# Kernel optimization log

Measured on AMD Instinct MI355X. Metric: run time of the kernel, lower is better.

The kernel has to match this reference:

```python
import jax, jax.numpy as jnp
import numpy as np

K, N, NE, NI, MA, IN, B = 8, 512, 256, 256, 3, 128, 1024
H, UNFOLDS = 0.04, 6
DT = H / UNFOLDS
STATE = NE * MA + NI * MA + NE + NI + N  # 2560


def inv_softplus(x):
    return float(np.log(np.expm1(x)))


def piecewise_sigmoid(x, S_a=0.9, S_c=0.0):
    a = S_a / 2.0
    c = S_c
    k = 0.5 / (1.0 - 2.0 * a)  # = 5.0 for S_a=0.9
    x1, x2, x3, x4 = c + a - 1.0, c - a, c + a, c + 1.0 - a
    quad_rise = k * (x - x1) * (x - x1)
    linear = x - c + 0.5
    quad_cap = 1.0 - k * (x - x4) * (x - x4)
    out = jnp.where(x < x1, 0.0, quad_rise)
    out = jnp.where(x >= x2, linear, out)
    out = jnp.where(x > x3, quad_cap, out)
    out = jnp.where(x > x4, 1.0, out)
    return out


def setup_inputs():
    key = jax.random.key(0)
    ks = jax.random.split(key, 6)
    m = (jax.random.uniform(ks[0], (K, N, N)) > 0.5).astype(jnp.float32)  # sparsity masks
    W_raw = jax.random.normal(ks[1], (K, N, N)) * np.float32(np.sqrt(2.0 / N)) * m
    W_in = jax.random.normal(ks[2], (K, N, IN)) * 0.1
    lo, hi = inv_softplus(0.25), inv_softplus(10.0)
    taus = jnp.asarray([lo + (hi - lo) * ai / (MA - 1) for ai in range(MA)], dtype=jnp.float32)
    log_tau_a = jnp.tile(taus[None, None, :], (K, NE, 1))
    return {
        "inputs": jax.random.normal(ks[3], (B, IN), dtype=jnp.float32),
        "state": jax.random.uniform(ks[4], (K, B, STATE), dtype=jnp.float32),
        "W_raw": W_raw,
        "sparsity_masks": m,
        "W_in": W_in,
        "a_0": jnp.full((K, N), 0.35, jnp.float32),
        "log_tau_d": jnp.full((K, N), inv_softplus(0.1), jnp.float32),
        "log_tau_a_E": log_tau_a,
        "log_c_E": jnp.full((K, NE, MA), -3.0, jnp.float32),
        "c_0_E": jnp.zeros((K, NE, MA), jnp.float32),
        "log_tau_a_I": log_tau_a,
        "log_c_I": jnp.full((K, NI, MA), -3.0, jnp.float32),
        "c_0_I": jnp.zeros((K, NI, MA), jnp.float32),
        "log_tau_b_rec_E": jnp.full((K, NE), inv_softplus(1.0), jnp.float32),
        "log_tau_b_rel_E": jnp.full((K, NE), inv_softplus(0.25), jnp.float32),
        "log_tau_b_rec_I": jnp.full((K, NI), inv_softplus(1.0), jnp.float32),
        "log_tau_b_rel_I": jnp.full((K, NI), inv_softplus(0.25), jnp.float32),
        "readout_ids": jnp.zeros((K,), dtype=jnp.int32),  # 0=synaptic,1=rate,2=dendritic
    }


def _forward(inputs, state, W_raw, sparsity_masks, W_in, a_0, log_tau_d,
             log_tau_a_E, log_c_E, c_0_E, log_tau_a_I, log_c_I, c_0_I,
             log_tau_b_rec_E, log_tau_b_rel_E, log_tau_b_rec_I, log_tau_b_rel_I,
             readout_ids):
    sp = jax.nn.softplus
    # unpack flat state (K,B,STATE)
    i0 = NE * MA; i1 = i0 + NI * MA; i2 = i1 + NE; i3 = i2 + NI
    aE = state[:, :, :i0].reshape(K, B, NE, MA)
    aI = state[:, :, i0:i1].reshape(K, B, NI, MA)
    bE = state[:, :, i1:i2]          # (K,B,NE)
    bI = state[:, :, i2:i3]          # (K,B,NI)
    x = state[:, :, i3:]             # (K,B,N)
    # Dale-constrained effective recurrent weights
    W_pos = sp(W_raw)
    W_eff = jnp.concatenate([W_pos[:, :, :NE], -W_pos[:, :, NE:]], axis=2) * sparsity_masks
    # time-constant gains
    gx = DT / sp(log_tau_d)[:, None]                    # (K,1,N)
    gaE = DT / sp(log_tau_a_E)[:, None]                 # (K,1,NE,MA)
    gaI = DT / sp(log_tau_a_I)[:, None]
    cE = sp(log_c_E)[:, None]                           # (K,1,NE,MA)
    cI = sp(log_c_I)[:, None]
    grecE = (DT / sp(log_tau_b_rec_E))[:, None]         # (K,1,NE)
    grelE = (DT / sp(log_tau_b_rel_E))[:, None]
    grecI = (DT / sp(log_tau_b_rec_I))[:, None]
    grelI = (DT / sp(log_tau_b_rel_I))[:, None]
    in_cur = jnp.einsum('kni,bi->kbn', W_in, inputs)    # constant across unfolds

    def rate_syn(aE, aI, bE, bI, x):
        thr = a_0[:, None] + jnp.concatenate(
            [jnp.sum(aE + c_0_E[:, None], axis=-1),
             jnp.sum(aI + c_0_I[:, None], axis=-1)], axis=-1)
        r = piecewise_sigmoid(x - thr)                  # (K,B,N)
        s = r * jnp.concatenate([bE, bI], axis=-1)      # depression-scaled output
        return r, s

    def step(carry, _):
        aE, aI, bE, bI, x = carry
        r, s = rate_syn(aE, aI, bE, bI, x)
        rE, rI = r[..., :NE], r[..., NE:]
        syn = jnp.einsum('knm,kbm->kbn', W_eff, s) + in_cur
        x = (x + gx * syn) / (1.0 + gx)                 # semi-implicit Euler
        aE = (aE + gaE * cE * rE[..., None]) / (1.0 + gaE)
        aI = (aI + gaI * cI * rI[..., None]) / (1.0 + gaI)
        bE = (bE + grecE) / (1.0 + grecE + grelE * rE)
        bI = (bI + grecI) / (1.0 + grecI + grelI * rI)
        return (aE, aI, bE, bI, x), None

    (aE, aI, bE, bI, x), _ = jax.lax.scan(step, (aE, aI, bE, bI, x), None, length=UNFOLDS)
    r, s = rate_syn(aE, aI, bE, bI, x)
    rid = readout_ids[:, None, None]
    out = jnp.where(rid == 0, s, jnp.where(rid == 1, r, x))
    new_state = jnp.concatenate(
        [aE.reshape(K, B, -1), aI.reshape(K, B, -1), bE, bI, x], axis=-1)
    return out, new_state


def reference(inputs, state, W_raw, sparsity_masks, W_in, a_0, log_tau_d,
              log_tau_a_E, log_c_E, c_0_E, log_tau_a_I, log_c_I, c_0_I,
              log_tau_b_rec_E, log_tau_b_rel_E, log_tau_b_rec_I, log_tau_b_rel_I,
              readout_ids):
    return _forward(inputs, state, W_raw, sparsity_masks, W_in, a_0, log_tau_d,
                    log_tau_a_E, log_c_E, c_0_E, log_tau_a_I, log_c_I, c_0_I,
                    log_tau_b_rec_E, log_tau_b_rel_E, log_tau_b_rec_I, log_tau_b_rel_I,
                    readout_ids)
```

## Files before the change

kernel.cpp:

```cpp
#include <hip/hip_runtime.h>
#include <stdint.h>

#define K_ 8
#define N_ 512
#define NE_ 256
#define MA_ 3
#define IN_ 128
#define B_ 1024
#define STATE_ 2560
#define UNFOLDS_ 6
#define DT_ (0.04f / 6.0f)

typedef __attribute__((ext_vector_type(8))) short short8;
typedef __attribute__((ext_vector_type(4))) float floatx4;

__device__ __forceinline__ float b2f(uint16_t u) {
    union { uint32_t i; float f; } v; v.i = ((uint32_t)u) << 16; return v.f;
}
__device__ __forceinline__ uint16_t f2b(float f) {
    union { float f; uint32_t i; } v; v.f = f;
    uint32_t i = v.i;
    uint32_t r = i + 0x7FFFu + ((i >> 16) & 1u);
    return (uint16_t)(r >> 16);
}
__device__ __forceinline__ uint32_t pack2(uint16_t lo, uint16_t hi) {
    return (uint32_t)lo | ((uint32_t)hi << 16);
}
__device__ __forceinline__ float loadf(const void* p, size_t i, int f32) {
    return f32 ? ((const float*)p)[i] : b2f(((const uint16_t*)p)[i]);
}
__device__ __forceinline__ float ntloadf(const void* p, size_t i, int f32) {
    return f32 ? __builtin_nontemporal_load((const float*)p + i)
               : b2f(__builtin_nontemporal_load((const uint16_t*)p + i));
}
__device__ __forceinline__ float spf(float x) {
    return (x > 20.f) ? x : log1pf(expf(x));
}
__device__ __forceinline__ float psig(float x) {
    float t1 = x + 0.55f;
    float q1 = 5.f * t1 * t1;
    float t2 = x - 0.55f;
    float q2 = 1.f - 5.f * t2 * t2;
    float out = (x < -0.55f) ? 0.f : q1;
    out = (x >= -0.45f) ? (x + 0.5f) : out;
    out = (x > 0.45f) ? q2 : out;
    out = (x > 0.55f) ? 1.f : out;
    return out;
}

__global__ void srnn_detect_kernel(const uint16_t* canary, int* flag) {
    __shared__ int cnt;
    if (threadIdx.x == 0) cnt = 0;
    __syncthreads();
    int bad = 0;
    for (int i = threadIdx.x; i < 4096; i += 256) {
        uint16_t u = canary[i];
        int e = (u >> 7) & 0xFF;
        if (e >= 0xC0) bad++;
    }
    atomicAdd(&cnt, bad);
    __syncthreads();
    if (threadIdx.x == 0) flag[0] = (cnt >= 16) ? 1 : 0;
}

__global__ void srnn_params_kernel(
    const void* a0, const void* ltd,
    const void* ltaE, const void* lcE, const void* c0E,
    const void* ltaI, const void* lcI, const void* c0I,
    const void* lbrecE, const void* lbrelE,
    const void* lbrecI, const void* lbrelI,
    const int* flag, float* P)
{
    const int f = flag[0];
    int idx = blockIdx.x * 256 + threadIdx.x;
    if (idx >= K_ * N_) return;
    int n = idx & (N_ - 1);
    int k = idx >> 9;
    float gx = DT_ / spf(loadf(ltd, idx, f));
    float thr0 = loadf(a0, idx, f);

    const void *lta, *lc, *c0, *lbrec, *lbrel;
    int nn;
    if (n < NE_) { nn = n;        lta = ltaE; lc = lcE; c0 = c0E; lbrec = lbrecE; lbrel = lbrelE; }
    else         { nn = n - NE_;  lta = ltaI; lc = lcI; c0 = c0I; lbrec = lbrecI; lbrel = lbrelI; }
    int base3 = (k * NE_ + nn) * MA_;
    int base1 = k * NE_ + nn;

    float amul[3], ainv[3];
    #pragma unroll
    for (int j = 0; j < 3; ++j) {
        float ga = DT_ / spf(loadf(lta, base3 + j, f));
        float c  = spf(loadf(lc, base3 + j, f));
        amul[j] = ga * c;
        ainv[j] = 1.f / (1.f + ga);
        thr0 += loadf(c0, base3 + j, f);
    }
    float grec = DT_ / spf(loadf(lbrec, base1, f));
    float grel = DT_ / spf(loadf(lbrel, base1, f));

    const int KN = K_ * N_;
    P[0*KN + idx] = gx;
    P[1*KN + idx] = 1.f / (1.f + gx);
    P[2*KN + idx] = thr0;
    P[3*KN + idx] = grec;
    P[4*KN + idx] = grel;
    P[5*KN + idx] = amul[0]; P[6*KN + idx] = amul[1]; P[7*KN + idx] = amul[2];
    P[8*KN + idx] = ainv[0]; P[9*KN + idx] = ainv[1]; P[10*KN + idx] = ainv[2];
    P[11*KN + idx] = 1.f + grec;
}

__global__ __launch_bounds__(256) void srnn_wsw_kernel(
    const void* __restrict__ Wraw, const void* __restrict__ mask,
    const int* __restrict__ flag, uint16_t* __restrict__ Wsw)
{
    __shared__ float tile[16 * 516];
    const int f = flag[0];
    const int nt = blockIdx.x, k = blockIdx.y, t = threadIdx.x;
    const size_t base = (size_t)k * N_ * N_ + (size_t)nt * 16 * N_;
    #pragma unroll
    for (int i = 0; i < 32; ++i) {
        int idx = i * 256 + t;
        int row = idx >> 9, m = idx & 511;
        size_t gi = base + (size_t)row * N_ + m;
        float w = spf(ntloadf(Wraw, gi, f)) * ntloadf(mask, gi, f);
        if (m >= NE_) w = -w;
        tile[row * 516 + m] = w;
    }
    __syncthreads();
    uint16_t* outb = Wsw + ((size_t)k * 32 + nt) * (16 * 64 * 8);
    #pragma unroll
    for (int i = 0; i < 4; ++i) {
        int id = i * 256 + t;
        int ks = id >> 6, L = id & 63;
        int row = L & 15, quad = L >> 4;
        const float* src = &tile[row * 516 + ks * 32 + quad * 8];
        uint4 v;
        v.x = pack2(f2b(src[0]), f2b(src[1]));
        v.y = pack2(f2b(src[2]), f2b(src[3]));
        v.z = pack2(f2b(src[4]), f2b(src[5]));
        v.w = pack2(f2b(src[6]), f2b(src[7]));
        *(uint4*)(outb + (size_t)id * 8) = v;
    }
}

__global__ __launch_bounds__(256) void srnn_winsw_kernel(
    const void* __restrict__ Win, const int* __restrict__ flag,
    uint16_t* __restrict__ Winsw)
{
    __shared__ float tile[16 * 132];
    const int f = flag[0];
    const int nt = blockIdx.x, k = blockIdx.y, t = threadIdx.x;
    const size_t base = (size_t)k * N_ * IN_ + (size_t)nt * 16 * IN_;
    #pragma unroll
    for (int i = 0; i < 8; ++i) {
        int idx = i * 256 + t;
        int row = idx >> 7, c = idx & 127;
        tile[row * 132 + c] = ntloadf(Win, base + (size_t)row * IN_ + c, f);
    }
    __syncthreads();
    uint16_t* outb = Winsw + ((size_t)k * 32 + nt) * (4 * 64 * 8);
    {
        int id = t;
        int ks = id >> 6, L = id & 63;
        int row = L & 15, quad = L >> 4;
        const float* src = &tile[row * 132 + ks * 32 + quad * 8];
        uint4 v;
        v.x = pack2(f2b(src[0]), f2b(src[1]));
        v.y = pack2(f2b(src[2]), f2b(src[3]));
        v.z = pack2(f2b(src[4]), f2b(src[5]));
        v.w = pack2(f2b(src[6]), f2b(src[7]));
        *(uint4*)(outb + (size_t)id * 8) = v;
    }
}

__global__ __launch_bounds__(1024, 4)
void srnn_main_kernel(const void* __restrict__ state,
                      const void* __restrict__ inputs,
                      const uint16_t* __restrict__ Wsw,
                      const uint16_t* __restrict__ Winsw,
                      const float* __restrict__ P,
                      const int* __restrict__ readout,
                      const int* __restrict__ flag,
                      void* __restrict__ out)
{
    __shared__ __align__(16) uint16_t sT[2][16 * 520];
    __shared__ __align__(16) float xL[2][16 * 516];
    __shared__ __align__(16) uint16_t icL[2][16 * 520];
    __shared__ __align__(16) float Pl[12 * 512];

    const int f = flag[0];
    const int t = threadIdx.x;
    const int k = blockIdx.x & 7;
    const int b0 = (blockIdx.x >> 3) * 32;
    const int sub = t >> 9;
    const int n = t & 511;
    const int lane = t & 63, w = t >> 6;
    const int bq = lane & 15, quad = lane >> 4;

    {
        const int KN = K_ * N_;
        #pragma unroll
        for (int q = 0; q < 6; ++q) {
            int idx = q * 1024 + t;
            Pl[idx] = P[(idx >> 9) * KN + k * N_ + (idx & 511)];
        }
    }
    #pragma unroll
    for (int q = 0; q < 4; ++q) {
        int idx = q * 1024 + t;
        int ss = idx >> 11, rem = idx & 2047;
        int bb = rem >> 7, ii = rem & 127;
        (ss ? sT[1] : sT[0])[bb * 136 + ii] =
            f2b(ntloadf(inputs, (size_t)(b0 + ss * 16 + bb) * IN_ + ii, f));
    }
    float a0v[16], a1v[16], a2v[16], bv[16];
    #pragma unroll
    for (int bb = 0; bb < 16; ++bb) {
        size_t sb = ((size_t)k * B_ + b0 + sub * 16 + bb) * STATE_;
        a0v[bb] = ntloadf(state, sb + 3 * n + 0, f);
        a1v[bb] = ntloadf(state, sb + 3 * n + 1, f);
        a2v[bb] = ntloadf(state, sb + 3 * n + 2, f);
        bv[bb]  = ntloadf(state, sb + 1536 + n, f);
        xL[sub][bb * 516 + n] = ntloadf(state, sb + 2048 + n, f);
    }
    __syncthreads();

    const uint16_t* bpe0 = sT[0] + bq * 520 + quad * 8;
    const uint16_t* bpe1 = sT[1] + bq * 520 + quad * 8;
    const uint16_t* ape  = Wsw + (size_t)k * 262144 + (size_t)(2 * w) * 8192
                               + (size_t)lane * 8;
    const int nb0 = w * 32 + quad * 4;
    const int nb1 = nb0 + 16;

    {
        const uint16_t* upe0 = sT[0] + bq * 136 + quad * 8;
        const uint16_t* upe1 = sT[1] + bq * 136 + quad * 8;
        const uint16_t* apie = Winsw + (size_t)(k * 32 + 2 * w) * 2048
                                     + (size_t)lane * 8;
        floatx4 c00 = {0.f,0.f,0.f,0.f}, c01 = c00, c10 = c00, c11 = c00;
        #pragma unroll
        for (int e = 0; e < 4; ++e) {
            short8 bu0 = *(const short8*)(upe0 + e * 32);
            short8 bu1 = *(const short8*)(upe1 + e * 32);
            short8 aw0 = *(const short8*)(apie + e * 512);
            short8 aw1 = *(const short8*)(apie + 2048 + e * 512);
            c00 = __builtin_amdgcn_mfma_f32_16x16x32_bf16(aw0, bu0, c00, 0, 0, 0);
            c01 = __builtin_amdgcn_mfma_f32_16x16x32_bf16(aw0, bu1, c01, 0, 0, 0);
            c10 = __builtin_amdgcn_mfma_f32_16x16x32_bf16(aw1, bu0, c10, 0, 0, 0);
            c11 = __builtin_amdgcn_mfma_f32_16x16x32_bf16(aw1, bu1, c11, 0, 0, 0);
        }
        uint2 pv;
        pv.x = pack2(f2b(c00[0]), f2b(c00[1])); pv.y = pack2(f2b(c00[2]), f2b(c00[3]));
        *(uint2*)(icL[0] + bq * 520 + nb0) = pv;
        pv.x = pack2(f2b(c01[0]), f2b(c01[1])); pv.y = pack2(f2b(c01[2]), f2b(c01[3]));
        *(uint2*)(icL[1] + bq * 520 + nb0) = pv;
        pv.x = pack2(f2b(c10[0]), f2b(c10[1])); pv.y = pack2(f2b(c10[2]), f2b(c10[3]));
        *(uint2*)(icL[0] + bq * 520 + nb1) = pv;
        pv.x = pack2(f2b(c11[0]), f2b(c11[1])); pv.y = pack2(f2b(c11[2]), f2b(c11[3]));
        *(uint2*)(icL[1] + bq * 520 + nb1) = pv;
    }
    __syncthreads();

    for (int step = 0; step < UNFOLDS_; ++step) {
        {
            const float thr0 = Pl[2*512+n], grec = Pl[3*512+n], grel = Pl[4*512+n];
            const float am0 = Pl[5*512+n], am1 = Pl[6*512+n], am2 = Pl[7*512+n];
            const float ai0 = Pl[8*512+n], ai1 = Pl[9*512+n], ai2 = Pl[10*512+n];
            const float ogr = Pl[11*512+n];
            #pragma unroll
            for (int bb = 0; bb < 16; ++bb) {
                float x = xL[sub][bb * 516 + n];
                float thr = thr0 + a0v[bb] + a1v[bb] + a2v[bb];
                float r = psig(x - thr);
                float s = r * bv[bb];
                a0v[bb] = fmaf(am0, r, a0v[bb]) * ai0;
                a1v[bb] = fmaf(am1, r, a1v[bb]) * ai1;
                a2v[bb] = fmaf(am2, r, a2v[bb]) * ai2;
                bv[bb] = (bv[bb] + grec) *
                         __builtin_amdgcn_rcpf(fmaf(grel, r, ogr));
                sT[sub][bb * 520 + n] = f2b(s);
            }
        }
        __syncthreads();

        {
            floatx4 c00 = {0.f,0.f,0.f,0.f}, c01 = c00, c10 = c00, c11 = c00;
            #pragma unroll 2
            for (int ks = 0; ks < 16; ++ks) {
                short8 bf0 = *(const short8*)(bpe0 + ks * 32);
                short8 bf1 = *(const short8*)(bpe1 + ks * 32);
                short8 af0 = *(const short8*)(ape + ks * 512);
                short8 af1 = *(const short8*)(ape + 8192 + ks * 512);
                c00 = __builtin_amdgcn_mfma_f32_16x16x32_bf16(af0, bf0, c00, 0, 0, 0);
                c01 = __builtin_amdgcn_mfma_f32_16x16x32_bf16(af0, bf1, c01, 0, 0, 0);
                c10 = __builtin_amdgcn_mfma_f32_16x16x32_bf16(af1, bf0, c10, 0, 0, 0);
                c11 = __builtin_amdgcn_mfma_f32_16x16x32_bf16(af1, bf1, c11, 0, 0, 0);
            }
            uint2 q00 = *(const uint2*)(icL[0] + bq * 520 + nb0);
            uint2 q01 = *(const uint2*)(icL[1] + bq * 520 + nb0);
            uint2 q10 = *(const uint2*)(icL[0] + bq * 520 + nb1);
            uint2 q11 = *(const uint2*)(icL[1] + bq * 520 + nb1);
            floatx4 i00 = {b2f((uint16_t)q00.x), b2f((uint16_t)(q00.x >> 16)),
                           b2f((uint16_t)q00.y), b2f((uint16_t)(q00.y >> 16))};
            floatx4 i01 = {b2f((uint16_t)q01.x), b2f((uint16_t)(q01.x >> 16)),
                           b2f((uint16_t)q01.y), b2f((uint16_t)(q01.y >> 16))};
            floatx4 i10 = {b2f((uint16_t)q10.x), b2f((uint16_t)(q10.x >> 16)),
                           b2f((uint16_t)q10.y), b2f((uint16_t)(q10.y >> 16))};
            floatx4 i11 = {b2f((uint16_t)q11.x), b2f((uint16_t)(q11.x >> 16)),
                           b2f((uint16_t)q11.y), b2f((uint16_t)(q11.y >> 16))};
            floatx4 g0  = *(const floatx4*)&Pl[0*512 + nb0];
            floatx4 iv0 = *(const floatx4*)&Pl[1*512 + nb0];
            floatx4 g1  = *(const floatx4*)&Pl[0*512 + nb1];
            floatx4 iv1 = *(const floatx4*)&Pl[1*512 + nb1];
            float* p00 = &xL[0][bq * 516 + nb0];
            float* p01 = &xL[1][bq * 516 + nb0];
            float* p10 = &xL[0][bq * 516 + nb1];
            float* p11 = &xL[1][bq * 516 + nb1];
            floatx4 v;
            v = *(floatx4*)p00; v = (v + g0 * (c00 + i00)) * iv0; *(floatx4*)p00 = v;
            v = *(floatx4*)p01; v = (v + g0 * (c01 + i01)) * iv0; *(floatx4*)p01 = v;
            v = *(floatx4*)p10; v = (v + g1 * (c10 + i10)) * iv1; *(floatx4*)p10 = v;
            v = *(floatx4*)p11; v = (v + g1 * (c11 + i11)) * iv1; *(floatx4*)p11 = v;
        }
        __syncthreads();
    }

    const int rid = readout[k];
    const float thr0e = Pl[2*512+n];
    if (f) {
        float* outp = (float*)out;
        float* nst = outp + (size_t)K_ * B_ * N_;
        #pragma unroll
        for (int bb = 0; bb < 16; ++bb) {
            float x = xL[sub][bb * 516 + n];
            float thr = thr0e + a0v[bb] + a1v[bb] + a2v[bb];
            float r = psig(x - thr);
            float s = r * bv[bb];
            float o = (rid == 0) ? s : ((rid == 1) ? r : x);
            size_t ob = (size_t)k * B_ + b0 + sub * 16 + bb;
            __builtin_nontemporal_store(o, outp + ob * N_ + n);
            float* st = nst + ob * STATE_;
            __builtin_nontemporal_store(a0v[bb], st + 3 * n + 0);
            __builtin_nontemporal_store(a1v[bb], st + 3 * n + 1);
            __builtin_nontemporal_store(a2v[bb], st + 3 * n + 2);
            __builtin_nontemporal_store(bv[bb], st + 1536 + n);
            __builtin_nontemporal_store(x, st + 2048 + n);
        }
    } else {
        uint16_t* outp = (uint16_t*)out;
        uint16_t* nst = outp + (size_t)K_ * B_ * N_;
        #pragma unroll
        for (int bb = 0; bb < 16; ++bb) {
            float x = xL[sub][bb * 516 + n];
            float thr = thr0e + a0v[bb] + a1v[bb] + a2v[bb];
            float r = psig(x - thr);
            float s = r * bv[bb];
            float o = (rid == 0) ? s : ((rid == 1) ? r : x);
            size_t ob = (size_t)k * B_ + b0 + sub * 16 + bb;
            __builtin_nontemporal_store(f2b(o), outp + ob * N_ + n);
            uint16_t* st = nst + ob * STATE_;
            __builtin_nontemporal_store(f2b(a0v[bb]), st + 3 * n + 0);
            __builtin_nontemporal_store(f2b(a1v[bb]), st + 3 * n + 1);
            __builtin_nontemporal_store(f2b(a2v[bb]), st + 3 * n + 2);
            __builtin_nontemporal_store(f2b(bv[bb]), st + 1536 + n);
            __builtin_nontemporal_store(f2b(x), st + 2048 + n);
        }
    }
}

extern "C" void kernel_launch(void* const* d_in, const int* in_sizes, int n_in,
                              void* d_out, int out_size, void* d_ws, size_t ws_size,
                              hipStream_t stream) {
    const void* inputs = d_in[0];
    const void* state  = d_in[1];
    const void* Wraw   = d_in[2];
    const void* mask   = d_in[3];
    const void* Win    = d_in[4];
    const void* a0     = d_in[5];
    const void* ltd    = d_in[6];
    const void* ltaE   = d_in[7];
    const void* lcE    = d_in[8];
    const void* c0E    = d_in[9];
    const void* ltaI   = d_in[10];
    const void* lcI    = d_in[11];
    const void* c0I    = d_in[12];
    const void* lbrecE = d_in[13];
    const void* lbrelE = d_in[14];
    const void* lbrecI = d_in[15];
    const void* lbrelI = d_in[16];
    const int* readout = (const int*)d_in[17];

    char* ws = (char*)d_ws;
    int* flag       = (int*)ws;
    float* P        = (float*)(ws + 256);
    uint16_t* Wsw   = (uint16_t*)(ws + 256 + 196608);
    uint16_t* Winsw = (uint16_t*)(ws + 256 + 196608 + 4194304);

    srnn_detect_kernel<<<dim3(1), dim3(256), 0, stream>>>((const uint16_t*)Wraw, flag);
    srnn_params_kernel<<<dim3(16), dim3(256), 0, stream>>>(
        a0, ltd, ltaE, lcE, c0E, ltaI, lcI, c0I, lbrecE, lbrelE, lbrecI, lbrelI, flag, P);
    srnn_wsw_kernel<<<dim3(32, 8), dim3(256), 0, stream>>>(Wraw, mask, flag, Wsw);
    srnn_winsw_kernel<<<dim3(32, 8), dim3(256), 0, stream>>>(Win, flag, Winsw);
    srnn_main_kernel<<<dim3(256), dim3(1024), 0, stream>>>(
        state, inputs, Wsw, Winsw, P, readout, flag, d_out);
}
```

Before: 330.4 us.

## Pack per-thread recurrent state into bf16 pairs and use hardware bf16 conversion

Stores the four per-batch recurrent state values (three adaptation terms and the synaptic resource) as packed bf16 pairs in 32 registers instead of 64 fp32 registers. The goal is to cut register pressure and raise occupancy. It also swaps the software round-to-nearest bf16 conversion for the v_cvt_pk_bf16_f32 instruction. The cost is precision: the state is rounded to bf16 after every unfold step, so error builds up across steps and fp32 outputs lose accuracy compared with the reference.

```diff
diff --git a/kernel.cpp b/kernel.cpp
--- a/kernel.cpp
+++ b/kernel.cpp
@@ -25,6 +25,17 @@
 }
 __device__ __forceinline__ uint32_t pack2(uint16_t lo, uint16_t hi) {
     return (uint32_t)lo | ((uint32_t)hi << 16);
+}
+__device__ __forceinline__ uint32_t cvtpk(float lo, float hi) {
+    uint32_t r;
+    asm("v_cvt_pk_bf16_f32 %0, %1, %2" : "=v"(r) : "v"(lo), "v"(hi));
+    return r;
+}
+__device__ __forceinline__ float lo16f(uint32_t u) {
+    union { uint32_t i; float f; } v; v.i = u << 16; return v.f;
+}
+__device__ __forceinline__ float hi16f(uint32_t u) {
+    union { uint32_t i; float f; } v; v.i = u & 0xFFFF0000u; return v.f;
 }
 __device__ __forceinline__ float loadf(const void* p, size_t i, int f32) {
     return f32 ? ((const float*)p)[i] : b2f(((const uint16_t*)p)[i]);
@@ -213,14 +224,14 @@
         (ss ? sT[1] : sT[0])[bb * 136 + ii] =
             f2b(ntloadf(inputs, (size_t)(b0 + ss * 16 + bb) * IN_ + ii, f));
     }
-    float a0v[16], a1v[16], a2v[16], bv[16];
+    uint32_t pa[16], pb[16];
     #pragma unroll
     for (int bb = 0; bb < 16; ++bb) {
         size_t sb = ((size_t)k * B_ + b0 + sub * 16 + bb) * STATE_;
-        a0v[bb] = ntloadf(state, sb + 3 * n + 0, f);
-        a1v[bb] = ntloadf(state, sb + 3 * n + 1, f);
-        a2v[bb] = ntloadf(state, sb + 3 * n + 2, f);
-        bv[bb]  = ntloadf(state, sb + 1536 + n, f);
+        pa[bb] = cvtpk(ntloadf(state, sb + 3 * n + 0, f),
+                       ntloadf(state, sb + 3 * n + 1, f));
+        pb[bb] = cvtpk(ntloadf(state, sb + 3 * n + 2, f),
+                       ntloadf(state, sb + 1536 + n, f));
         xL[sub][bb * 516 + n] = ntloadf(state, sb + 2048 + n, f);
     }
     __syncthreads();
@@ -250,13 +261,13 @@
             c11 = __builtin_amdgcn_mfma_f32_16x16x32_bf16(aw1, bu1, c11, 0, 0, 0);
         }
         uint2 pv;
-        pv.x = pack2(f2b(c00[0]), f2b(c00[1])); pv.y = pack2(f2b(c00[2]), f2b(c00[3]));
+        pv.x = cvtpk(c00[0], c00[1]); pv.y = cvtpk(c00[2], c00[3]);
         *(uint2*)(icL[0] + bq * 520 + nb0) = pv;
-        pv.x = pack2(f2b(c01[0]), f2b(c01[1])); pv.y = pack2(f2b(c01[2]), f2b(c01[3]));
+        pv.x = cvtpk(c01[0], c01[1]); pv.y = cvtpk(c01[2], c01[3]);
         *(uint2*)(icL[1] + bq * 520 + nb0) = pv;
-        pv.x = pack2(f2b(c10[0]), f2b(c10[1])); pv.y = pack2(f2b(c10[2]), f2b(c10[3]));
+        pv.x = cvtpk(c10[0], c10[1]); pv.y = cvtpk(c10[2], c10[3]);
         *(uint2*)(icL[0] + bq * 520 + nb1) = pv;
-        pv.x = pack2(f2b(c11[0]), f2b(c11[1])); pv.y = pack2(f2b(c11[2]), f2b(c11[3]));
+        pv.x = cvtpk(c11[0], c11[1]); pv.y = cvtpk(c11[2], c11[3]);
         *(uint2*)(icL[1] + bq * 520 + nb1) = pv;
     }
     __syncthreads();
@@ -270,15 +281,18 @@
             #pragma unroll
             for (int bb = 0; bb < 16; ++bb) {
                 float x = xL[sub][bb * 516 + n];
-                float thr = thr0 + a0v[bb] + a1v[bb] + a2v[bb];
+                float a0 = lo16f(pa[bb]), a1 = hi16f(pa[bb]);
+                float a2 = lo16f(pb[bb]), bv = hi16f(pb[bb]);
+                float thr = thr0 + a0 + a1 + a2;
                 float r = psig(x - thr);
-                float s = r * bv[bb];
-                a0v[bb] = fmaf(am0, r, a0v[bb]) * ai0;
-                a1v[bb] = fmaf(am1, r, a1v[bb]) * ai1;
-                a2v[bb] = fmaf(am2, r, a2v[bb]) * ai2;
-                bv[bb] = (bv[bb] + grec) *
-                         __builtin_amdgcn_rcpf(fmaf(grel, r, ogr));
-                sT[sub][bb * 520 + n] = f2b(s);
+                float s = r * bv;
+                a0 = fmaf(am0, r, a0) * ai0;
+                a1 = fmaf(am1, r, a1) * ai1;
+                a2 = fmaf(am2, r, a2) * ai2;
+                bv = (bv + grec) * __builtin_amdgcn_rcpf(fmaf(grel, r, ogr));
+                pa[bb] = cvtpk(a0, a1);
+                pb[bb] = cvtpk(a2, bv);
+                sT[sub][bb * 520 + n] = (uint16_t)cvtpk(s, s);
             }
         }
         __syncthreads();
@@ -300,14 +314,10 @@
             uint2 q01 = *(const uint2*)(icL[1] + bq * 520 + nb0);
             uint2 q10 = *(const uint2*)(icL[0] + bq * 520 + nb1);
             uint2 q11 = *(const uint2*)(icL[1] + bq * 520 + nb1);
-            floatx4 i00 = {b2f((uint16_t)q00.x), b2f((uint16_t)(q00.x >> 16)),
-                           b2f((uint16_t)q00.y), b2f((uint16_t)(q00.y >> 16))};
-            floatx4 i01 = {b2f((uint16_t)q01.x), b2f((uint16_t)(q01.x >> 16)),
-                           b2f((uint16_t)q01.y), b2f((uint16_t)(q01.y >> 16))};
-            floatx4 i10 = {b2f((uint16_t)q10.x), b2f((uint16_t)(q10.x >> 16)),
-                           b2f((uint16_t)q10.y), b2f((uint16_t)(q10.y >> 16))};
-            floatx4 i11 = {b2f((uint16_t)q11.x), b2f((uint16_t)(q11.x >> 16)),
-                           b2f((uint16_t)q11.y), b2f((uint16_t)(q11.y >> 16))};
+            floatx4 i00 = {lo16f(q00.x), hi16f(q00.x), lo16f(q00.y), hi16f(q00.y)};
+            floatx4 i01 = {lo16f(q01.x), hi16f(q01.x), lo16f(q01.y), hi16f(q01.y)};
+            floatx4 i10 = {lo16f(q10.x), hi16f(q10.x), lo16f(q10.y), hi16f(q10.y)};
+            floatx4 i11 = {lo16f(q11.x), hi16f(q11.x), lo16f(q11.y), hi16f(q11.y)};
             floatx4 g0  = *(const floatx4*)&Pl[0*512 + nb0];
             floatx4 iv0 = *(const floatx4*)&Pl[1*512 + nb0];
             floatx4 g1  = *(const floatx4*)&Pl[0*512 + nb1];
@@ -333,17 +343,19 @@
         #pragma unroll
         for (int bb = 0; bb < 16; ++bb) {
             float x = xL[sub][bb * 516 + n];
-            float thr = thr0e + a0v[bb] + a1v[bb] + a2v[bb];
+            float a0 = lo16f(pa[bb]), a1 = hi16f(pa[bb]);
+            float a2 = lo16f(pb[bb]), bv = hi16f(pb[bb]);
+            float thr = thr0e + a0 + a1 + a2;
             float r = psig(x - thr);
-            float s = r * bv[bb];
+            float s = r * bv;
             float o = (rid == 0) ? s : ((rid == 1) ? r : x);
             size_t ob = (size_t)k * B_ + b0 + sub * 16 + bb;
             __builtin_nontemporal_store(o, outp + ob * N_ + n);
             float* st = nst + ob * STATE_;
-            __builtin_nontemporal_store(a0v[bb], st + 3 * n + 0);
-            __builtin_nontemporal_store(a1v[bb], st + 3 * n + 1);
-            __builtin_nontemporal_store(a2v[bb], st + 3 * n + 2);
-            __builtin_nontemporal_store(bv[bb], st + 1536 + n);
+            __builtin_nontemporal_store(a0, st + 3 * n + 0);
+            __builtin_nontemporal_store(a1, st + 3 * n + 1);
+            __builtin_nontemporal_store(a2, st + 3 * n + 2);
+            __builtin_nontemporal_store(bv, st + 1536 + n);
             __builtin_nontemporal_store(x, st + 2048 + n);
         }
     } else {
@@ -352,17 +364,19 @@
         #pragma unroll
         for (int bb = 0; bb < 16; ++bb) {
             float x = xL[sub][bb * 516 + n];
-            float thr = thr0e + a0v[bb] + a1v[bb] + a2v[bb];
+            float a0 = lo16f(pa[bb]), a1 = hi16f(pa[bb]);
+            float a2 = lo16f(pb[bb]), bv = hi16f(pb[bb]);
+            float thr = thr0e + a0 + a1 + a2;
             float r = psig(x - thr);
-            float s = r * bv[bb];
+            float s = r * bv;
             float o = (rid == 0) ? s : ((rid == 1) ? r : x);
             size_t ob = (size_t)k * B_ + b0 + sub * 16 + bb;
             __builtin_nontemporal_store(f2b(o), outp + ob * N_ + n);
             uint16_t* st = nst + ob * STATE_;
-            __builtin_nontemporal_store(f2b(a0v[bb]), st + 3 * n + 0);
-            __builtin_nontemporal_store(f2b(a1v[bb]), st + 3 * n + 1);
-            __builtin_nontemporal_store(f2b(a2v[bb]), st + 3 * n + 2);
-            __builtin_nontemporal_store(f2b(bv[bb]), st + 1536 + n);
+            __builtin_nontemporal_store((uint16_t)pa[bb], st + 3 * n + 0);
+            __builtin_nontemporal_store((uint16_t)(pa[bb] >> 16), st + 3 * n + 1);
+            __builtin_nontemporal_store((uint16_t)pb[bb], st + 3 * n + 2);
+            __builtin_nontemporal_store((uint16_t)(pb[bb] >> 16), st + 1536 + n);
             __builtin_nontemporal_store(f2b(x), st + 2048 + n);
         }
     }
```

Result: no change. 335.3 us (+1.5%).
